# Optimization experiments

Measured on AMD Instinct MI355X. Metric: run time of the kernel, lower is better.

Reference implementation:

```python
import jax, jax.numpy as jnp
import numpy as np

K = 6                      # max_displacement / pad_size
WIN = 2 * K + 1            # displacement window side
D = WIN * WIN              # number of affinity channels (169)


def setup_inputs() -> dict:
    key = jax.random.key(0)
    k1, k2 = jax.random.split(key)
    aff = jax.random.normal(k1, (4, D, 192, 192), dtype=jnp.float32)
    input2 = jax.random.normal(k2, (4, 64, 192, 192), dtype=jnp.float32)
    return {"aff": aff, "input2": input2}


def reference(aff, input2):
    # output[b,c,y,x] = sum_{dy,dx in [-k,k]} aff[b, idx(dy,dx), y, x]
    #                   * input2_zeropad[b, c, y+dy, x+dx]
    # Scanned over the (2k+1)^2 displacements to avoid materializing the
    # [B, D, C, H, W] cost-volume intermediate.
    B, C, H, W = input2.shape
    Dn = aff.shape[1]
    win = int(round(Dn ** 0.5))
    k = (win - 1) // 2
    padded = jnp.pad(input2, ((0, 0), (0, 0), (k, k), (k, k)))  # [B,C,H+2k,W+2k]
    aff_t = jnp.transpose(aff, (1, 0, 2, 3))  # [D,B,H,W]
    ds = jnp.arange(Dn)

    def body(acc, xs):
        d, a = xs                      # a: [B,H,W]
        dy = d // win                  # 0..2k (offset into padded rows)
        dx = d % win                   # 0..2k (offset into padded cols)
        patch = jax.lax.dynamic_slice(padded, (0, 0, dy, dx), (B, C, H, W))
        return acc + a[:, None, :, :] * patch, None

    out, _ = jax.lax.scan(body, jnp.zeros_like(input2), (ds, aff_t))
    return out
```

## Files before the change

kernel.cpp:

```cpp
#include <hip/hip_runtime.h>


#define KD   6
#define WIN  13
#define ND   169
#define NB   4
#define NC   64
#define NH   192
#define NW   192
#define HW   (NH * NW)
#define XH   64
#define PITCHW 42
#define BUFW (NC * PITCHW)
#define AFFPW 448
#define NTH  256

typedef _Float16 half2v __attribute__((ext_vector_type(2)));

static __device__ __forceinline__ half2v h2(unsigned u) {
    return __builtin_bit_cast(half2v, u);
}
static __device__ __forceinline__ unsigned pk(float a, float b) {
    return __builtin_bit_cast(unsigned, __builtin_amdgcn_cvt_pkrtz(a, b));
}

#if __has_builtin(__builtin_amdgcn_fdot2)
#define FDOT2(a, b, c) __builtin_amdgcn_fdot2((a), (b), (c), false)
#else
static __device__ __forceinline__ float fdot2_fb(half2v a, half2v b, float c) {
    return fmaf((float)a.x, (float)b.x, fmaf((float)a.y, (float)b.y, c));
}
#define FDOT2(a, b, c) fdot2_fb((a), (b), (c))
#endif

__global__ __launch_bounds__(NTH)
__attribute__((amdgpu_waves_per_eu(4, 8)))
void mxassemble(const float* __restrict__ aff,
                const float* __restrict__ in2,
                float* __restrict__ out) {
    __shared__ unsigned ldsw[2 * BUFW];
    __shared__ unsigned apkw[2 * AFFPW];

    const int bx = blockIdx.x;
    const int g  = bx & 7;
    const int k  = bx >> 3;
    const int b  = k / 24;
    const int yl = k - 24 * b;
    const int y  = 24 * g + yl;
    const int xb = blockIdx.y;
    const int X0 = xb * XH;

    const int t    = threadIdx.x;
    const int l    = t & 63;
    const int wv   = t >> 6;
    const int cg   = l & 15;
    const int xs   = l >> 4;
    const int slot = wv * 4 + xs;
    const int x0   = X0 + slot * 4;

    if (xb != 1) {
        const int w0 = (xb == 0) ? 0 : 36;
        if (t < NC * 2) {
            const int c = t >> 1, qq = t & 1;
            *(uint2*)&ldsw[c * PITCHW + w0 + 2 * qq]        = make_uint2(0u, 0u);
            *(uint2*)&ldsw[BUFW + c * PITCHW + w0 + 2 * qq] = make_uint2(0u, 0u);
        }
    }

    int wadr[5], goff[5];
#pragma unroll
    for (int s = 0; s < 5; ++s) {
        const int ii = t + NTH * s;
        const int c  = ii / 20;
        const int q  = ii - 20 * c;
        const int xg = X0 - 8 + 4 * q;
        const bool ok = (xg >= 0) && (xg < NW);
        wadr[s] = ok ? (c * PITCHW + 2 * q) : -1;
        goff[s] = c * HW + xg;
    }

    const int am  = t >> 4;
    const int axc = t & 15;
    const bool astg = (t < 112);
    const float* pA0 = aff + (size_t)b * ND * HW + (size_t)y * NW + X0
                           + 4 * axc + (size_t)(2 * am) * HW;
    const int aw = am * 64 + 4 * axc;

    float acc[4][4];
#pragma unroll
    for (int i = 0; i < 4; ++i)
#pragma unroll
        for (int j = 0; j < 4; ++j) acc[i][j] = 0.f;

    const float* in2_b = in2 + (size_t)b * NC * HW;
    const int wbase = cg * PITCHW + 2 * slot;

    if (astg) {
        const float4 A0 = *(const float4*)pA0;
        float4 A1 = make_float4(0.f, 0.f, 0.f, 0.f);
        if (am < 6) A1 = *(const float4*)(pA0 + HW);
        uint4 w;
        w.x = pk(A0.x, A1.x); w.y = pk(A0.y, A1.y);
        w.z = pk(A0.z, A1.z); w.w = pk(A0.w, A1.w);
        *(uint4*)&apkw[aw] = w;
    }
    {
        const int r0 = y - KD;
        if (r0 >= 0) {
            const float* p = in2_b + (size_t)r0 * NW;
            float4 Sv[5];
#pragma unroll
            for (int s = 0; s < 5; ++s)
                if (wadr[s] >= 0) Sv[s] = *(const float4*)&p[goff[s]];
#pragma unroll
            for (int s = 0; s < 5; ++s)
                if (wadr[s] >= 0) {
                    uint2 w; w.x = pk(Sv[s].x, Sv[s].y); w.y = pk(Sv[s].z, Sv[s].w);
                    *(uint2*)&ldsw[wadr[s]] = w;
                }
        }
    }
    __syncthreads();

    for (int rr = 0; rr < WIN; ++rr) {
        const unsigned* cur  = ldsw + ((rr & 1) ? BUFW : 0);
        unsigned*       nxt  = ldsw + ((rr & 1) ? 0 : BUFW);
        const unsigned* acur = apkw + ((rr & 1) ? AFFPW : 0) + 4 * slot;
        unsigned*       anxt = apkw + ((rr & 1) ? 0 : AFFPW);
        const int  r  = y - KD + rr;
        const bool pv = (r >= 0) && (r < NH);
        const int  rn = r + 1;
        const bool sv = (rr < WIN - 1) && (rn >= 0) && (rn < NH);

        float4 A0, A1;
        const bool av = astg && (rr < WIN - 1);
        if (av) {
            const float* p = pA0 + (size_t)((rr + 1) * WIN) * HW;
            A0 = *(const float4*)p;
            A1 = make_float4(0.f, 0.f, 0.f, 0.f);
            if (am < 6) A1 = *(const float4*)(p + HW);
            asm volatile("" : "+v"(A0.x), "+v"(A0.y), "+v"(A0.z), "+v"(A0.w));
            asm volatile("" : "+v"(A1.x), "+v"(A1.y), "+v"(A1.z), "+v"(A1.w));
        }
        float4 Sv[5];
        if (sv) {
            const float* p = in2_b + (size_t)rn * NW;
#pragma unroll
            for (int s = 0; s < 5; ++s)
                if (wadr[s] >= 0) Sv[s] = *(const float4*)&p[goff[s]];
#pragma unroll
            for (int s = 0; s < 5; ++s)
                asm volatile("" : "+v"(Sv[s].x), "+v"(Sv[s].y),
                                  "+v"(Sv[s].z), "+v"(Sv[s].w));
        }
        __builtin_amdgcn_sched_barrier(0);

        if (pv) {
            unsigned W[4][10];
#pragma unroll
            for (int i = 0; i < 4; ++i) {
                const unsigned* wp = cur + wbase + i * (16 * PITCHW);
                *(uint2*)&W[i][0] = *(const uint2*)&wp[0];
                *(uint2*)&W[i][2] = *(const uint2*)&wp[2];
                *(uint2*)&W[i][4] = *(const uint2*)&wp[4];
                *(uint2*)&W[i][6] = *(const uint2*)&wp[6];
                *(uint2*)&W[i][8] = *(const uint2*)&wp[8];
            }
#pragma unroll
            for (int m = 0; m < 7; ++m) {
                unsigned A4[4];
                *(uint4*)&A4[0] = *(const uint4*)&acur[m * 64];
#pragma unroll
                for (int i = 0; i < 4; ++i) {
                    const unsigned p1 = W[i][m + 1];
                    const unsigned p2 = W[i][m + 2];
                    const unsigned p3 = W[i][m + 3];
                    const unsigned s1 = (p1 >> 16) | (p2 << 16);
                    const unsigned s2 = (p2 >> 16) | (p3 << 16);
                    acc[i][0] = FDOT2(h2(A4[0]), h2(p1), acc[i][0]);
                    acc[i][1] = FDOT2(h2(A4[1]), h2(s1), acc[i][1]);
                    acc[i][2] = FDOT2(h2(A4[2]), h2(p2), acc[i][2]);
                    acc[i][3] = FDOT2(h2(A4[3]), h2(s2), acc[i][3]);
                }
            }
        }

        if (av) {
            uint4 w;
            w.x = pk(A0.x, A1.x); w.y = pk(A0.y, A1.y);
            w.z = pk(A0.z, A1.z); w.w = pk(A0.w, A1.w);
            *(uint4*)&anxt[aw] = w;
        }
        if (sv) {
#pragma unroll
            for (int s = 0; s < 5; ++s)
                if (wadr[s] >= 0) {
                    uint2 w; w.x = pk(Sv[s].x, Sv[s].y); w.y = pk(Sv[s].z, Sv[s].w);
                    *(uint2*)&nxt[wadr[s]] = w;
                }
        }

        __syncthreads();
    }

    float* ob = out + (((size_t)b * NC + cg) * NH + y) * NW + x0;
#pragma unroll
    for (int i = 0; i < 4; ++i) {
        *(float4*)&ob[(size_t)(16 * i) * HW] =
            make_float4(acc[i][0], acc[i][1], acc[i][2], acc[i][3]);
    }
}

extern "C" void kernel_launch(void* const* d_in, const int* in_sizes, int n_in,
                              void* d_out, int out_size, void* d_ws, size_t ws_size,
                              hipStream_t stream) {
    const float* aff = (const float*)d_in[0];
    const float* in2 = (const float*)d_in[1];
    float* outp = (float*)d_out;
    dim3 grid(NB * NH, 3, 1);
    dim3 block(NTH);
    hipLaunchKernelGGL(mxassemble, grid, block, 0, stream, aff, in2, outp);
}
```

Measured before the change: 260.6 us.

## Prefetch affinity two rows ahead and software-pipeline LDS reads in inner loop

Affinity loads are now issued two displacement rows ahead and held in registers across an iteration, giving global loads more time to land before they are packed into LDS. The inner compute splits the four channel groups into two halves, loads their LDS windows in batches, and prefetches the next affinity vector from LDS while the current dot products run. __syncthreads is replaced by an inline-asm wait on lgkmcnt plus s_barrier, so the barrier does not wait for outstanding global loads. This costs extra VGPRs for the held registers, which may reduce occupancy.

```diff
diff --git a/kernel.cpp b/kernel.cpp
--- a/kernel.cpp
+++ b/kernel.cpp
@@ -33,6 +33,10 @@
 #define FDOT2(a, b, c) fdot2_fb((a), (b), (c))
 #endif
 
+#define BARRIER() asm volatile("s_waitcnt lgkmcnt(0)\n\ts_barrier" ::: "memory")
+#define PINF4(v) asm volatile("" : "+v"((v).x), "+v"((v).y), "+v"((v).z), "+v"((v).w))
+#define PINU4(v) asm volatile("" : "+v"((v).x), "+v"((v).y), "+v"((v).z), "+v"((v).w))
+
 __global__ __launch_bounds__(NTH)
 __attribute__((amdgpu_waves_per_eu(4, 8)))
 void mxassemble(const float* __restrict__ aff,
@@ -95,14 +99,21 @@
     const float* in2_b = in2 + (size_t)b * NC * HW;
     const int wbase = cg * PITCHW + 2 * slot;
 
+    float4 Ap0 = make_float4(0.f, 0.f, 0.f, 0.f), Ap1 = Ap0;
+    float4 An0 = Ap0, An1 = Ap0;
+
     if (astg) {
-        const float4 A0 = *(const float4*)pA0;
-        float4 A1 = make_float4(0.f, 0.f, 0.f, 0.f);
-        if (am < 6) A1 = *(const float4*)(pA0 + HW);
+        const float4 a0 = *(const float4*)pA0;
+        float4 a1 = make_float4(0.f, 0.f, 0.f, 0.f);
+        if (am < 6) a1 = *(const float4*)(pA0 + HW);
         uint4 w;
-        w.x = pk(A0.x, A1.x); w.y = pk(A0.y, A1.y);
-        w.z = pk(A0.z, A1.z); w.w = pk(A0.w, A1.w);
+        w.x = pk(a0.x, a1.x); w.y = pk(a0.y, a1.y);
+        w.z = pk(a0.z, a1.z); w.w = pk(a0.w, a1.w);
         *(uint4*)&apkw[aw] = w;
+        const float* p = pA0 + (size_t)WIN * HW;
+        Ap0 = *(const float4*)p;
+        if (am < 6) Ap1 = *(const float4*)(p + HW);
+        PINF4(Ap0); PINF4(Ap1);
     }
     {
         const int r0 = y - KD;
@@ -120,7 +131,7 @@
                 }
         }
     }
-    __syncthreads();
+    BARRIER();
 
     for (int rr = 0; rr < WIN; ++rr) {
         const unsigned* cur  = ldsw + ((rr & 1) ? BUFW : 0);
@@ -131,16 +142,15 @@
         const bool pv = (r >= 0) && (r < NH);
         const int  rn = r + 1;
         const bool sv = (rr < WIN - 1) && (rn >= 0) && (rn < NH);
-
-        float4 A0, A1;
-        const bool av = astg && (rr < WIN - 1);
-        if (av) {
-            const float* p = pA0 + (size_t)((rr + 1) * WIN) * HW;
-            A0 = *(const float4*)p;
-            A1 = make_float4(0.f, 0.f, 0.f, 0.f);
-            if (am < 6) A1 = *(const float4*)(p + HW);
-            asm volatile("" : "+v"(A0.x), "+v"(A0.y), "+v"(A0.z), "+v"(A0.w));
-            asm volatile("" : "+v"(A1.x), "+v"(A1.y), "+v"(A1.z), "+v"(A1.w));
+        const bool al = astg && (rr <= 10);
+        const bool ap = astg && (rr <= 11);
+
+        if (al) {
+            const float* p = pA0 + (size_t)((rr + 2) * WIN) * HW;
+            An0 = *(const float4*)p;
+            An1 = make_float4(0.f, 0.f, 0.f, 0.f);
+            if (am < 6) An1 = *(const float4*)(p + HW);
+            PINF4(An0); PINF4(An1);
         }
         float4 Sv[5];
         if (sv) {
@@ -150,47 +160,76 @@
                 if (wadr[s] >= 0) Sv[s] = *(const float4*)&p[goff[s]];
 #pragma unroll
             for (int s = 0; s < 5; ++s)
-                asm volatile("" : "+v"(Sv[s].x), "+v"(Sv[s].y),
-                                  "+v"(Sv[s].z), "+v"(Sv[s].w));
+                PINF4(Sv[s]);
         }
         __builtin_amdgcn_sched_barrier(0);
 
         if (pv) {
-            unsigned W[4][10];
-#pragma unroll
-            for (int i = 0; i < 4; ++i) {
-                const unsigned* wp = cur + wbase + i * (16 * PITCHW);
-                *(uint2*)&W[i][0] = *(const uint2*)&wp[0];
-                *(uint2*)&W[i][2] = *(const uint2*)&wp[2];
-                *(uint2*)&W[i][4] = *(const uint2*)&wp[4];
-                *(uint2*)&W[i][6] = *(const uint2*)&wp[6];
-                *(uint2*)&W[i][8] = *(const uint2*)&wp[8];
-            }
-#pragma unroll
-            for (int m = 0; m < 7; ++m) {
-                unsigned A4[4];
-                *(uint4*)&A4[0] = *(const uint4*)&acur[m * 64];
-#pragma unroll
-                for (int i = 0; i < 4; ++i) {
-                    const unsigned p1 = W[i][m + 1];
-                    const unsigned p2 = W[i][m + 2];
-                    const unsigned p3 = W[i][m + 3];
-                    const unsigned s1 = (p1 >> 16) | (p2 << 16);
-                    const unsigned s2 = (p2 >> 16) | (p3 << 16);
-                    acc[i][0] = FDOT2(h2(A4[0]), h2(p1), acc[i][0]);
-                    acc[i][1] = FDOT2(h2(A4[1]), h2(s1), acc[i][1]);
-                    acc[i][2] = FDOT2(h2(A4[2]), h2(p2), acc[i][2]);
-                    acc[i][3] = FDOT2(h2(A4[3]), h2(s2), acc[i][3]);
+#pragma unroll
+            for (int h = 0; h < 2; ++h) {
+                unsigned Wa[10], Wb[10];
+                const unsigned* wpa = cur + wbase + (2*h + 0) * (16 * PITCHW);
+                const unsigned* wpb = cur + wbase + (2*h + 1) * (16 * PITCHW);
+                *(uint2*)&Wa[0] = *(const uint2*)&wpa[0];
+                *(uint2*)&Wa[2] = *(const uint2*)&wpa[2];
+                *(uint2*)&Wa[4] = *(const uint2*)&wpa[4];
+                *(uint2*)&Wa[6] = *(const uint2*)&wpa[6];
+                *(uint2*)&Wa[8] = *(const uint2*)&wpa[8];
+                *(uint2*)&Wb[0] = *(const uint2*)&wpb[0];
+                *(uint2*)&Wb[2] = *(const uint2*)&wpb[2];
+                *(uint2*)&Wb[4] = *(const uint2*)&wpb[4];
+                *(uint2*)&Wb[6] = *(const uint2*)&wpb[6];
+                *(uint2*)&Wb[8] = *(const uint2*)&wpb[8];
+                asm volatile("" : "+v"(Wa[0]), "+v"(Wa[1]), "+v"(Wa[2]),
+                                  "+v"(Wa[3]), "+v"(Wa[4]), "+v"(Wa[5]),
+                                  "+v"(Wa[6]), "+v"(Wa[7]), "+v"(Wa[8]),
+                                  "+v"(Wa[9]));
+                asm volatile("" : "+v"(Wb[0]), "+v"(Wb[1]), "+v"(Wb[2]),
+                                  "+v"(Wb[3]), "+v"(Wb[4]), "+v"(Wb[5]),
+                                  "+v"(Wb[6]), "+v"(Wb[7]), "+v"(Wb[8]),
+                                  "+v"(Wb[9]));
+                uint4 ac = *(const uint4*)&acur[0];
+#pragma unroll
+                for (int m = 0; m < 7; ++m) {
+                    uint4 an;
+                    if (m < 6) {
+                        an = *(const uint4*)&acur[(m + 1) * 64];
+                        PINU4(an);
+                    }
+                    {
+                        const unsigned p1 = Wa[m + 1];
+                        const unsigned p2 = Wa[m + 2];
+                        const unsigned p3 = Wa[m + 3];
+                        const unsigned s1 = (p1 >> 16) | (p2 << 16);
+                        const unsigned s2 = (p2 >> 16) | (p3 << 16);
+                        acc[2*h][0] = FDOT2(h2(ac.x), h2(p1), acc[2*h][0]);
+                        acc[2*h][1] = FDOT2(h2(ac.y), h2(s1), acc[2*h][1]);
+                        acc[2*h][2] = FDOT2(h2(ac.z), h2(p2), acc[2*h][2]);
+                        acc[2*h][3] = FDOT2(h2(ac.w), h2(s2), acc[2*h][3]);
+                    }
+                    {
+                        const unsigned p1 = Wb[m + 1];
+                        const unsigned p2 = Wb[m + 2];
+                        const unsigned p3 = Wb[m + 3];
+                        const unsigned s1 = (p1 >> 16) | (p2 << 16);
+                        const unsigned s2 = (p2 >> 16) | (p3 << 16);
+                        acc[2*h+1][0] = FDOT2(h2(ac.x), h2(p1), acc[2*h+1][0]);
+                        acc[2*h+1][1] = FDOT2(h2(ac.y), h2(s1), acc[2*h+1][1]);
+                        acc[2*h+1][2] = FDOT2(h2(ac.z), h2(p2), acc[2*h+1][2]);
+                        acc[2*h+1][3] = FDOT2(h2(ac.w), h2(s2), acc[2*h+1][3]);
+                    }
+                    if (m < 6) ac = an;
                 }
             }
         }
 
-        if (av) {
+        if (ap) {
             uint4 w;
-            w.x = pk(A0.x, A1.x); w.y = pk(A0.y, A1.y);
-            w.z = pk(A0.z, A1.z); w.w = pk(A0.w, A1.w);
+            w.x = pk(Ap0.x, Ap1.x); w.y = pk(Ap0.y, Ap1.y);
+            w.z = pk(Ap0.z, Ap1.z); w.w = pk(Ap0.w, Ap1.w);
             *(uint4*)&anxt[aw] = w;
         }
+        if (al) { Ap0 = An0; Ap1 = An1; }
         if (sv) {
 #pragma unroll
             for (int s = 0; s < 5; ++s)
@@ -200,7 +239,7 @@
                 }
         }
 
-        __syncthreads();
+        BARRIER();
     }
 
     float* ob = out + (((size_t)b * NC + cg) * NH + y) * NW + x0;
```

Result: no change. 263.1 us (+1.0%).
